# Kernel optimization log

Measured on AMD Instinct MI355X. Metric: run time of the kernel, lower is better.

The kernel has to match this reference:

```python
import jax, jax.numpy as jnp
import numpy as np


def setup_inputs() -> dict:
    key = jax.random.key(0)
    k1, k2, k3 = jax.random.split(key, 3)
    B, Na, Nb = 64, 8192, 8192
    phases_a = jax.random.normal(k1, (B, Na), dtype=jnp.float32)
    phases_b = jax.random.normal(k2, (B, Nb), dtype=jnp.float32)
    # Binary coupled-pair indicator mask (N_a, N_b)
    coupling_mask = jax.random.randint(k3, (Na, Nb), 0, 2, dtype=jnp.int32)
    return {"phases_a": phases_a, "phases_b": phases_b, "coupling_mask": coupling_mask}


def reference(phases_a, phases_b, coupling_mask):
    """Masked phase-locking value (PLV) between two oscillator banks.

    Mathematically identical to |sum_ij M_ij * exp(i*(a_i - b_j))| / sum(M),
    but computed via trig identities + matmul instead of materializing the
    O(B*Na*Nb) complex tensor:
      real = sum_ij M_ij (cos a_i cos b_j + sin a_i sin b_j)
      imag = sum_ij M_ij (sin a_i cos b_j - cos a_i sin b_j)
    """
    ca, sa = jnp.cos(phases_a), jnp.sin(phases_a)   # (B, Na)
    cb, sb = jnp.cos(phases_b), jnp.sin(phases_b)   # (B, Nb)
    M = coupling_mask.astype(ca.dtype)              # (Na, Nb)
    caM = ca @ M                                    # (B, Nb)
    saM = sa @ M                                    # (B, Nb)
    real = jnp.sum(caM * cb + saM * sb, axis=-1)    # (B,)
    imag = jnp.sum(saM * cb - caM * sb, axis=-1)    # (B,)
    n_pairs = jnp.maximum(M.sum(), jnp.asarray(1.0, ca.dtype))
    return jnp.sqrt(real * real + imag * imag) / n_pairs
```

## Files before the change

kernel.cpp:

```cpp
#include <hip/hip_runtime.h>
#include <hip/hip_bf16.h>

#define NA 8192
#define NB 8192
#define NBATCH 64
#define NC 128
#define BM 128
#define WM 32
#define SPLITK 8
#define KCHUNK (NB / SPLITK)
#define NBLK (SPLITK * NA / BM)

#define XT_BYTES (NC * NB * 2)
#define CTR_OFF  XT_BYTES
#define PBLK_OFF (CTR_OFF + 512)

typedef __bf16 bf16x8 __attribute__((ext_vector_type(8)));
typedef float  f32x4  __attribute__((ext_vector_type(4)));
typedef int    ivec4  __attribute__((ext_vector_type(4)));

__global__ __launch_bounds__(256) void prep_b_kernel(
    const float* __restrict__ pb, __hip_bfloat16* __restrict__ Xtf,
    int* __restrict__ count)
{
    int tid = blockIdx.x * 256 + threadIdx.x;
    if (tid == 0) *count = 0;

    int b = tid >> 13;
    int k = tid & (NB - 1);

    float ph = pb[tid];
    float s, c;
    __sincosf(ph, &s, &c);

    int kstep = k >> 5;
    int quad  = (k >> 3) & 3;
    int e     = k & 7;
    int t     = b >> 3;
    int m0    = (2 * b) & 15;
    size_t base = ((size_t)(kstep * 8 + t) * 64 + quad * 16) * 8 + e;
    Xtf[base + (size_t)m0 * 8]       = __float2bfloat16(c);
    Xtf[base + (size_t)(m0 + 1) * 8] = __float2bfloat16(s);
}

__global__ __launch_bounds__(256, 2) void gemm_kernel(
    const int* __restrict__ mask, const __hip_bfloat16* __restrict__ Xtfg,
    const float* __restrict__ pa,
    float* __restrict__ Pblk, int* __restrict__ count)
{
    const int tid  = threadIdx.x;
    const int wave = tid >> 6;
    const int lane = tid & 63;
    const int quad = lane >> 4;
    const int m    = lane & 15;
    const int itile = blockIdx.x;
    const int kc    = blockIdx.y;
    const int k0    = kc * KCHUNK;

    const int rowbase = itile * BM + wave * WM;
    const bf16x8* __restrict__ xf = reinterpret_cast<const bf16x8*>(Xtfg);

    f32x4 acc[2][8];
#pragma unroll
    for (int f = 0; f < 2; ++f)
#pragma unroll
        for (int t = 0; t < 8; ++t)
            acc[f][t] = (f32x4){0.f, 0.f, 0.f, 0.f};

    int cnt = 0;

    for (int kk = k0; kk < k0 + KCHUNK; kk += 32) {
        const int kq = kk + quad * 8;

        bf16x8 a[2];
#pragma unroll
        for (int f = 0; f < 2; ++f) {
            const ivec4* p = reinterpret_cast<const ivec4*>(
                mask + (size_t)(rowbase + f * 16 + m) * NB + kq);
            ivec4 r0 = __builtin_nontemporal_load(p);
            ivec4 r1 = __builtin_nontemporal_load(p + 1);
            cnt += r0.x + r0.y + r0.z + r0.w + r1.x + r1.y + r1.z + r1.w;
            uint4 u;
            u.x = (r0.x ? 0x3F80u : 0u) | (r0.y ? 0x3F800000u : 0u);
            u.y = (r0.z ? 0x3F80u : 0u) | (r0.w ? 0x3F800000u : 0u);
            u.z = (r1.x ? 0x3F80u : 0u) | (r1.y ? 0x3F800000u : 0u);
            u.w = (r1.z ? 0x3F80u : 0u) | (r1.w ? 0x3F800000u : 0u);
            a[f] = __builtin_bit_cast(bf16x8, u);
        }

        const bf16x8* fx = xf + (size_t)(kk >> 5) * 8 * 64 + lane;
#pragma unroll
        for (int t = 0; t < 8; ++t) {
            const bf16x8 bfrag = fx[t * 64];
            acc[0][t] = __builtin_amdgcn_mfma_f32_16x16x32_bf16(a[0], bfrag, acc[0][t], 0, 0, 0);
            acc[1][t] = __builtin_amdgcn_mfma_f32_16x16x32_bf16(a[1], bfrag, acc[1][t], 0, 0, 0);
        }
    }

    __shared__ float lred[4][64][2];
    const int odd = m & 1;

#pragma unroll
    for (int t = 0; t < 8; ++t) {
        const int b = t * 8 + (m >> 1);
        float rc = 0.f, ic = 0.f;
#pragma unroll
        for (int f = 0; f < 2; ++f)
#pragma unroll
            for (int r = 0; r < 4; ++r) {
                int row = rowbase + f * 16 + quad * 4 + r;
                float ph = pa[(size_t)b * NA + row];
                float sn, cs;
                __sincosf(ph, &sn, &cs);
                float Ax = odd ? sn : cs;
                float Bx = odd ? -cs : sn;
                rc = fmaf(Ax, acc[f][t][r], rc);
                ic = fmaf(Bx, acc[f][t][r], ic);
            }
        rc += __shfl_xor(rc, 1);  ic += __shfl_xor(ic, 1);
        rc += __shfl_xor(rc, 16); ic += __shfl_xor(ic, 16);
        rc += __shfl_xor(rc, 32); ic += __shfl_xor(ic, 32);
        if (quad == 0 && !odd) {
            lred[wave][b][0] = rc;
            lred[wave][b][1] = ic;
        }
    }
    __syncthreads();

    if (tid < 128) {
        float s = lred[0][tid >> 1][tid & 1] + lred[1][tid >> 1][tid & 1]
                + lred[2][tid >> 1][tid & 1] + lred[3][tid >> 1][tid & 1];
        int bid = blockIdx.y * 64 + blockIdx.x;
        Pblk[(size_t)bid * 128 + tid] = s;
    }

#pragma unroll
    for (int off = 32; off > 0; off >>= 1) cnt += __shfl_down(cnt, off);
    if (lane == 0) atomicAdd(count, cnt);
}

__global__ __launch_bounds__(512) void final_kernel(
    const float* __restrict__ Pblk, const int* __restrict__ count,
    float* __restrict__ out)
{
    const int t = threadIdx.x;
    const int grp = t & 3;
    const int idx = t >> 2;

    float s = 0.f;
#pragma unroll 8
    for (int blk = grp * (NBLK / 4); blk < (grp + 1) * (NBLK / 4); ++blk)
        s += Pblk[(size_t)blk * 128 + idx];
    s += __shfl_xor(s, 1);
    s += __shfl_xor(s, 2);

    __shared__ float red[128];
    if (grp == 0) red[idx] = s;
    __syncthreads();

    if (t < NBATCH) {
        float r = red[2 * t], im = red[2 * t + 1];
        float n = fmaxf((float)(*count), 1.0f);
        out[t] = sqrtf(r * r + im * im) / n;
    }
}

extern "C" void kernel_launch(void* const* d_in, const int* in_sizes, int n_in,
                              void* d_out, int out_size, void* d_ws, size_t ws_size,
                              hipStream_t stream) {
    const float* pa   = (const float*)d_in[0];
    const float* pb   = (const float*)d_in[1];
    const int*   mask = (const int*)d_in[2];
    float* out = (float*)d_out;

    char* ws = (char*)d_ws;
    __hip_bfloat16* Xtf = (__hip_bfloat16*)ws;
    int*   count = (int*)(ws + CTR_OFF);
    float* Pblk  = (float*)(ws + PBLK_OFF);

    prep_b_kernel<<<(NBATCH * NB) / 256, 256, 0, stream>>>(pb, Xtf, count);

    dim3 g(NA / BM, SPLITK);
    gemm_kernel<<<g, 256, 0, stream>>>(mask, Xtf, pa, Pblk, count);

    final_kernel<<<1, 512, 0, stream>>>(Pblk, count, out);
}
```

Baseline: 418.9 us.

## Double-buffer GEMM loads, popcount mask conversion, vectorize prep and final reduction

The GEMM main loop is unrolled by two with register double-buffering, so mask and B-fragment loads for the next k-step are issued before the MFMAs of the current one. Mask-to-bf16 conversion now packs pairs of ints, uses popcount for the pair count and a multiply for the bf16 ones. The prep kernel processes 8 elements per thread with vector stores. The final reduction is transposed and split across 64 blocks. The extra buffers raise register pressure, and the conversion assumes mask values are exactly 0 or 1.

Measured after the change: 410.2 us. -2.1%, faster.

```diff
diff --git a/kernel.cpp b/kernel.cpp
--- a/kernel.cpp
+++ b/kernel.cpp
@@ -18,6 +18,7 @@
 typedef __bf16 bf16x8 __attribute__((ext_vector_type(8)));
 typedef float  f32x4  __attribute__((ext_vector_type(4)));
 typedef int    ivec4  __attribute__((ext_vector_type(4)));
+typedef unsigned short u16x8 __attribute__((ext_vector_type(8)));
 
 __global__ __launch_bounds__(256) void prep_b_kernel(
     const float* __restrict__ pb, __hip_bfloat16* __restrict__ Xtf,
@@ -26,21 +27,53 @@
     int tid = blockIdx.x * 256 + threadIdx.x;
     if (tid == 0) *count = 0;
 
-    int b = tid >> 13;
-    int k = tid & (NB - 1);
-
-    float ph = pb[tid];
-    float s, c;
-    __sincosf(ph, &s, &c);
-
-    int kstep = k >> 5;
-    int quad  = (k >> 3) & 3;
-    int e     = k & 7;
+    int b  = tid >> 10;
+    int kg = tid & 1023;
+    int k  = kg << 3;
+
+    const float4* pp = reinterpret_cast<const float4*>(pb + ((size_t)b << 13) + k);
+    float4 v0 = pp[0], v1 = pp[1];
+    float ph[8] = {v0.x, v0.y, v0.z, v0.w, v1.x, v1.y, v1.z, v1.w};
+
+    u16x8 cv, sv;
+#pragma unroll
+    for (int e = 0; e < 8; ++e) {
+        float s, c;
+        __sincosf(ph[e], &s, &c);
+        cv[e] = __builtin_bit_cast(unsigned short, __float2bfloat16(c));
+        sv[e] = __builtin_bit_cast(unsigned short, __float2bfloat16(s));
+    }
+
+    int kstep = kg >> 2;
+    int quad  = kg & 3;
     int t     = b >> 3;
     int m0    = (2 * b) & 15;
-    size_t base = ((size_t)(kstep * 8 + t) * 64 + quad * 16) * 8 + e;
-    Xtf[base + (size_t)m0 * 8]       = __float2bfloat16(c);
-    Xtf[base + (size_t)(m0 + 1) * 8] = __float2bfloat16(s);
+    size_t base = (((size_t)(kstep * 8 + t) * 64) + quad * 16 + m0) * 8;
+    *reinterpret_cast<u16x8*>(&Xtf[base])     = cv;
+    *reinterpret_cast<u16x8*>(&Xtf[base + 8]) = sv;
+}
+
+struct Bfrags { bf16x8 v[8]; };
+
+__device__ __forceinline__ Bfrags load_b(const bf16x8* __restrict__ fx) {
+    Bfrags b;
+#pragma unroll
+    for (int t = 0; t < 8; ++t) b.v[t] = fx[t * 64];
+    return b;
+}
+
+__device__ __forceinline__ bf16x8 conv_a(ivec4 r0, ivec4 r1, int& cnt) {
+    unsigned p0 = (unsigned)r0.x | ((unsigned)r0.y << 16);
+    unsigned p1 = (unsigned)r0.z | ((unsigned)r0.w << 16);
+    unsigned p2 = (unsigned)r1.x | ((unsigned)r1.y << 16);
+    unsigned p3 = (unsigned)r1.z | ((unsigned)r1.w << 16);
+    cnt += __popc(p0) + __popc(p1) + __popc(p2) + __popc(p3);
+    uint4 u;
+    u.x = p0 * 0x3F80u;
+    u.y = p1 * 0x3F80u;
+    u.z = p2 * 0x3F80u;
+    u.w = p3 * 0x3F80u;
+    return __builtin_bit_cast(bf16x8, u);
 }
 
 __global__ __launch_bounds__(256, 2) void gemm_kernel(
@@ -69,31 +102,47 @@
 
     int cnt = 0;
 
-    for (int kk = k0; kk < k0 + KCHUNK; kk += 32) {
-        const int kq = kk + quad * 8;
-
-        bf16x8 a[2];
-#pragma unroll
-        for (int f = 0; f < 2; ++f) {
-            const ivec4* p = reinterpret_cast<const ivec4*>(
-                mask + (size_t)(rowbase + f * 16 + m) * NB + kq);
-            ivec4 r0 = __builtin_nontemporal_load(p);
-            ivec4 r1 = __builtin_nontemporal_load(p + 1);
-            cnt += r0.x + r0.y + r0.z + r0.w + r1.x + r1.y + r1.z + r1.w;
-            uint4 u;
-            u.x = (r0.x ? 0x3F80u : 0u) | (r0.y ? 0x3F800000u : 0u);
-            u.y = (r0.z ? 0x3F80u : 0u) | (r0.w ? 0x3F800000u : 0u);
-            u.z = (r1.x ? 0x3F80u : 0u) | (r1.y ? 0x3F800000u : 0u);
-            u.w = (r1.z ? 0x3F80u : 0u) | (r1.w ? 0x3F800000u : 0u);
-            a[f] = __builtin_bit_cast(bf16x8, u);
+    const int* mrow0 = mask + (size_t)(rowbase + m) * NB + quad * 8;
+    const int* mrow1 = mrow0 + (size_t)16 * NB;
+
+    auto load_a = [&](int kkk, ivec4& a00, ivec4& a01, ivec4& a10, ivec4& a11) {
+        const ivec4* p0 = reinterpret_cast<const ivec4*>(mrow0 + kkk);
+        a00 = __builtin_nontemporal_load(p0);
+        a01 = __builtin_nontemporal_load(p0 + 1);
+        const ivec4* p1 = reinterpret_cast<const ivec4*>(mrow1 + kkk);
+        a10 = __builtin_nontemporal_load(p1);
+        a11 = __builtin_nontemporal_load(p1 + 1);
+    };
+
+    ivec4 x00, x01, x10, x11;  Bfrags bx;
+    ivec4 y00, y01, y10, y11;  Bfrags by;
+
+    load_a(k0, x00, x01, x10, x11);
+    bx = load_b(xf + (size_t)(k0 >> 5) * 512 + lane);
+
+    for (int kk = k0; kk < k0 + KCHUNK; kk += 64) {
+        load_a(kk + 32, y00, y01, y10, y11);
+        by = load_b(xf + (size_t)((kk + 32) >> 5) * 512 + lane);
+        {
+            bf16x8 a0 = conv_a(x00, x01, cnt);
+            bf16x8 a1 = conv_a(x10, x11, cnt);
+#pragma unroll
+            for (int t = 0; t < 8; ++t) {
+                acc[0][t] = __builtin_amdgcn_mfma_f32_16x16x32_bf16(a0, bx.v[t], acc[0][t], 0, 0, 0);
+                acc[1][t] = __builtin_amdgcn_mfma_f32_16x16x32_bf16(a1, bx.v[t], acc[1][t], 0, 0, 0);
+            }
         }
-
-        const bf16x8* fx = xf + (size_t)(kk >> 5) * 8 * 64 + lane;
-#pragma unroll
-        for (int t = 0; t < 8; ++t) {
-            const bf16x8 bfrag = fx[t * 64];
-            acc[0][t] = __builtin_amdgcn_mfma_f32_16x16x32_bf16(a[0], bfrag, acc[0][t], 0, 0, 0);
-            acc[1][t] = __builtin_amdgcn_mfma_f32_16x16x32_bf16(a[1], bfrag, acc[1][t], 0, 0, 0);
+        const int kn = (kk + 64 < k0 + KCHUNK) ? (kk + 64) : k0;
+        load_a(kn, x00, x01, x10, x11);
+        bx = load_b(xf + (size_t)(kn >> 5) * 512 + lane);
+        {
+            bf16x8 a0 = conv_a(y00, y01, cnt);
+            bf16x8 a1 = conv_a(y10, y11, cnt);
+#pragma unroll
+            for (int t = 0; t < 8; ++t) {
+                acc[0][t] = __builtin_amdgcn_mfma_f32_16x16x32_bf16(a0, by.v[t], acc[0][t], 0, 0, 0);
+                acc[1][t] = __builtin_amdgcn_mfma_f32_16x16x32_bf16(a1, by.v[t], acc[1][t], 0, 0, 0);
+            }
         }
     }
 
@@ -131,7 +180,7 @@
         float s = lred[0][tid >> 1][tid & 1] + lred[1][tid >> 1][tid & 1]
                 + lred[2][tid >> 1][tid & 1] + lred[3][tid >> 1][tid & 1];
         int bid = blockIdx.y * 64 + blockIdx.x;
-        Pblk[(size_t)bid * 128 + tid] = s;
+        Pblk[(size_t)tid * NBLK + bid] = s;
     }
 
 #pragma unroll
@@ -139,29 +188,34 @@
     if (lane == 0) atomicAdd(count, cnt);
 }
 
-__global__ __launch_bounds__(512) void final_kernel(
+__global__ __launch_bounds__(256) void final_kernel(
     const float* __restrict__ Pblk, const int* __restrict__ count,
     float* __restrict__ out)
 {
+    const int b = blockIdx.x;
     const int t = threadIdx.x;
-    const int grp = t & 3;
-    const int idx = t >> 2;
-
-    float s = 0.f;
-#pragma unroll 8
-    for (int blk = grp * (NBLK / 4); blk < (grp + 1) * (NBLK / 4); ++blk)
-        s += Pblk[(size_t)blk * 128 + idx];
-    s += __shfl_xor(s, 1);
-    s += __shfl_xor(s, 2);
-
-    __shared__ float red[128];
-    if (grp == 0) red[idx] = s;
+
+    float r = 0.f, im = 0.f;
+#pragma unroll
+    for (int blk = t; blk < NBLK; blk += 256) {
+        r  += Pblk[(size_t)(2 * b)     * NBLK + blk];
+        im += Pblk[(size_t)(2 * b + 1) * NBLK + blk];
+    }
+#pragma unroll
+    for (int off = 32; off > 0; off >>= 1) {
+        r  += __shfl_down(r, off);
+        im += __shfl_down(im, off);
+    }
+
+    __shared__ float red[8];
+    if ((t & 63) == 0) { red[(t >> 6) * 2] = r; red[(t >> 6) * 2 + 1] = im; }
     __syncthreads();
 
-    if (t < NBATCH) {
-        float r = red[2 * t], im = red[2 * t + 1];
+    if (t == 0) {
+        float R = red[0] + red[2] + red[4] + red[6];
+        float I = red[1] + red[3] + red[5] + red[7];
         float n = fmaxf((float)(*count), 1.0f);
-        out[t] = sqrtf(r * r + im * im) / n;
+        out[b] = sqrtf(R * R + I * I) / n;
     }
 }
 
@@ -178,10 +232,10 @@
     int*   count = (int*)(ws + CTR_OFF);
     float* Pblk  = (float*)(ws + PBLK_OFF);
 
-    prep_b_kernel<<<(NBATCH * NB) / 256, 256, 0, stream>>>(pb, Xtf, count);
+    prep_b_kernel<<<(NBATCH * NB / 8) / 256, 256, 0, stream>>>(pb, Xtf, count);
 
     dim3 g(NA / BM, SPLITK);
     gemm_kernel<<<g, 256, 0, stream>>>(mask, Xtf, pa, Pblk, count);
 
-    final_kernel<<<1, 512, 0, stream>>>(Pblk, count, out);
-}
+    final_kernel<<<NBATCH, 256, 0, stream>>>(Pblk, count, out);
+}
```
